# Performance work log

Hardware: AMD Instinct MI355X
Metric: run time of the kernel (lower is better)

## Reference

```python
import jax, jax.numpy as jnp
import numpy as np

MAX_DEPTH = 8          # inner-node depths 1..8; leaves at depth 9
LMBDA = 0.1            # args.lmbda; per-node lmbda = LMBDA * 2**(-depth)
EPS = 1e-6


def setup_inputs() -> dict:
    key = jax.random.key(0)
    ks = jax.random.split(key, 7)
    B, D, O = 16384, 2048, 1000
    n_inner = 2 ** MAX_DEPTH - 1   # 255
    n_leaf = 2 ** MAX_DEPTH       # 256
    x = jax.random.normal(ks[0], (B, D), dtype=jnp.float32)
    target = jax.random.randint(ks[1], (B,), 0, O)
    y = jax.nn.one_hot(target, O, dtype=jnp.float32)  # target_onehot
    W = jax.random.normal(ks[2], (n_inner, D), dtype=jnp.float32) / np.sqrt(D)
    b = jax.random.normal(ks[3], (n_inner,), dtype=jnp.float32) * 0.01
    beta = jax.random.normal(ks[4], (n_inner,), dtype=jnp.float32)
    leaf_params = jax.random.normal(ks[5], (n_leaf, O), dtype=jnp.float32)
    return {"x": x, "y": y, "W": W, "b": b, "beta": beta, "leaf_params": leaf_params}


def reference(x, y, W, b, beta, leaf_params):
    """Faithful vectorized version of SoftDecisionTree.cal_loss.
    Inner nodes are stored in level-order (heap) layout, left-to-right
    within each level, matching the left-first recursion of cal_prob.
    Returns (loss, output) like cal_loss.
    """
    B = x.shape[0]
    dt = x.dtype
    # All inner-node gates in one fused GEMM: sigmoid(beta * (x @ w + b))
    probs = jax.nn.sigmoid(beta * (x @ W.T + b))  # [B, n_inner]

    path = jnp.ones((B, 1), dt)  # path_prob_init
    C = jnp.asarray(0.0, dt)
    idx = 0
    for d in range(1, MAX_DEPTH + 1):  # small fixed loop over tree levels
        n = 2 ** (d - 1)
        p = probs[:, idx:idx + n]      # gate probs for this level's nodes [B, n]
        if d < MAX_DEPTH:              # get_penalty skips nodes whose children are leaves
            denom = jnp.sum(path, axis=0)                  # [n]
            denom = jnp.where(denom == 0, EPS, denom)
            alpha = jnp.sum(p * path, axis=0) / denom      # [n]
            alpha = jnp.clip(alpha, EPS, 1.0 - EPS)
            lmbda = LMBDA * 2.0 ** (-d)
            C = C - jnp.sum(lmbda * 0.5 * (jnp.log(alpha) + jnp.log1p(-alpha)))
        # children: left gets path*(1-p), right gets path*p, interleaved
        path = jnp.stack([path * (1.0 - p), path * p], axis=-1).reshape(B, 2 * n)
        idx += n
    # path: [B, n_leaf] leaf arrival probabilities (left-to-right leaf order)

    logQ = jax.nn.log_softmax(leaf_params, axis=-1)  # [n_leaf, O]
    TQ = y @ logQ.T                                  # [B, n_leaf]: y . log Q per leaf
    loss_term = jnp.mean(jnp.sum(path * TQ, axis=1))
    loss = -loss_term + C

    best = jnp.argmax(path, axis=1)   # first max, matches the '<' update order
    output = jnp.exp(logQ)[best]      # [B, O] max_Q
    return loss, output
```

## Files before the change

kernel.cpp:

```cpp
#include <hip/hip_runtime.h>


typedef __attribute__((ext_vector_type(8))) short short8;
typedef __attribute__((ext_vector_type(4))) float f32x4;

#define B_ROWS 16384
#define DIM 2048
#define NCLS 1000
#define NINNER 255
#define NPAD 256

__device__ __forceinline__ unsigned cvt2bf(float a, float b) {
  return ((__float_as_uint(a) + 0x8000u) >> 16) | ((__float_as_uint(b) + 0x8000u) & 0xFFFF0000u);
}

__global__ __launch_bounds__(256) void prep_w(const float* __restrict__ W,
                                              const float* __restrict__ b,
                                              const float* __restrict__ beta,
                                              unsigned short* __restrict__ Wb,
                                              float* __restrict__ bp,
                                              float* __restrict__ betap) {
  int i = blockIdx.x * 256 + threadIdx.x;
  int n = i >> 11;
  float v = (n < NINNER) ? W[i] : 0.f;
  Wb[i] = (unsigned short)((__float_as_uint(v) + 0x8000u) >> 16);
  if (i < NPAD) {
    bp[i] = (i < NINNER) ? b[i] : 0.f;
    betap[i] = (i < NINNER) ? beta[i] : 0.f;
  }
}

__global__ __launch_bounds__(256) void leaf_softmax(const float* __restrict__ leaf,
                                                    float* __restrict__ logQ,
                                                    float* __restrict__ Q) {
  int l = blockIdx.x, t = threadIdx.x;
  const float* row = leaf + (size_t)l * NCLS;
  __shared__ float red[256];
  float mx = -3.4e38f;
  for (int j = t; j < NCLS; j += 256) mx = fmaxf(mx, row[j]);
  red[t] = mx; __syncthreads();
  for (int s = 128; s; s >>= 1) { if (t < s) red[t] = fmaxf(red[t], red[t + s]); __syncthreads(); }
  mx = red[0]; __syncthreads();
  float sm = 0.f;
  for (int j = t; j < NCLS; j += 256) sm += expf(row[j] - mx);
  red[t] = sm; __syncthreads();
  for (int s = 128; s; s >>= 1) { if (t < s) red[t] += red[t + s]; __syncthreads(); }
  float lse = mx + logf(red[0]);
  for (int j = t; j < NCLS; j += 256) {
    float lg = row[j] - lse;
    logQ[(size_t)l * NCLS + j] = lg;
    Q[(size_t)l * NCLS + j] = expf(lg);
  }
}

__global__ __launch_bounds__(256) void find_targets(const float* __restrict__ y,
                                                    int* __restrict__ tgt) {
  int wv = threadIdx.x >> 6, lane = threadIdx.x & 63;
  int r = blockIdx.x * 4 + wv;
  const float4* yr = (const float4*)(y + (size_t)r * NCLS);
  int found = 0x7fffffff;
#pragma unroll
  for (int i = 0; i < 4; ++i) {
    int j4 = i * 64 + lane;
    if (j4 < 250) {
      float4 v = yr[j4];
      if (v.x > 0.5f) found = min(found, 4 * j4 + 0);
      if (v.y > 0.5f) found = min(found, 4 * j4 + 1);
      if (v.z > 0.5f) found = min(found, 4 * j4 + 2);
      if (v.w > 0.5f) found = min(found, 4 * j4 + 3);
    }
  }
  for (int off = 32; off; off >>= 1) found = min(found, __shfl_down(found, off));
  if (lane == 0) tgt[r] = found;
}

__global__ __launch_bounds__(256) void gemm_probs(const float* __restrict__ x,
                                                  const unsigned short* __restrict__ Wb,
                                                  const float* __restrict__ bp,
                                                  const float* __restrict__ betap,
                                                  float* __restrict__ probs) {
  __shared__ __align__(16) unsigned short As[128 * 32];
  __shared__ __align__(16) unsigned short Bs[64 * 32];
  __shared__ float ep[128 * 65];
  __shared__ float bsh[64], besh[64];

  int tid = threadIdx.x;
  int lane = tid & 63, wave = tid >> 6;
  int m_base = blockIdx.x * 128;
  int n_base = blockIdx.y * 64;

  if (tid < 64) { bsh[tid] = bp[n_base + tid]; besh[tid] = betap[n_base + tid]; }

  f32x4 acc[2][4] = {};

  int arow = tid >> 1, ahalf = tid & 1;
  const float* aptr = x + (size_t)(m_base + arow) * DIM + ahalf * 16;
  unsigned short* asd = &As[arow * 32 + ahalf * 16];
  int brow = tid >> 2, bseg = tid & 3;
  const unsigned short* bptr = Wb + (size_t)(n_base + brow) * DIM + bseg * 8;
  unsigned short* bsd = &Bs[brow * 32 + bseg * 8];

  int frow = lane & 15, fquad = lane >> 4;
  const unsigned short* afrag0 = &As[(wave * 32 + frow) * 32 + fquad * 8];
  const unsigned short* afrag1 = afrag0 + 16 * 32;

  for (int kt = 0; kt < DIM; kt += 32) {
    float4 v0 = *(const float4*)(aptr + kt);
    float4 v1 = *(const float4*)(aptr + kt + 4);
    float4 v2 = *(const float4*)(aptr + kt + 8);
    float4 v3 = *(const float4*)(aptr + kt + 12);
    uint4 bw = *(const uint4*)(bptr + kt);
    uint4 p0, p1;
    p0.x = cvt2bf(v0.x, v0.y); p0.y = cvt2bf(v0.z, v0.w);
    p0.z = cvt2bf(v1.x, v1.y); p0.w = cvt2bf(v1.z, v1.w);
    p1.x = cvt2bf(v2.x, v2.y); p1.y = cvt2bf(v2.z, v2.w);
    p1.z = cvt2bf(v3.x, v3.y); p1.w = cvt2bf(v3.z, v3.w);
    __syncthreads();
    *(uint4*)asd = p0;
    *(uint4*)(asd + 8) = p1;
    *(uint4*)bsd = bw;
    __syncthreads();
    short8 a0 = *(const short8*)afrag0;
    short8 a1 = *(const short8*)afrag1;
#pragma unroll
    for (int nt = 0; nt < 4; ++nt) {
      short8 bfr = *(const short8*)&Bs[(nt * 16 + frow) * 32 + fquad * 8];
      acc[0][nt] = __builtin_amdgcn_mfma_f32_16x16x32_bf16(a0, bfr, acc[0][nt], 0, 0, 0);
      acc[1][nt] = __builtin_amdgcn_mfma_f32_16x16x32_bf16(a1, bfr, acc[1][nt], 0, 0, 0);
    }
  }
  __syncthreads();
#pragma unroll
  for (int mt = 0; mt < 2; ++mt)
#pragma unroll
    for (int nt = 0; nt < 4; ++nt)
#pragma unroll
      for (int rg = 0; rg < 4; ++rg)
        ep[(wave * 32 + mt * 16 + fquad * 4 + rg) * 65 + nt * 16 + frow] = acc[mt][nt][rg];
  __syncthreads();
  int mrow = tid >> 1, nh = (tid & 1) * 32;
  float* dst = probs + (size_t)(m_base + mrow) * NPAD + n_base + nh;
#pragma unroll
  for (int u = 0; u < 8; ++u) {
    int n0 = nh + u * 4;
    float4 o;
    o.x = 1.f / (1.f + expf(-besh[n0 + 0] * (ep[mrow * 65 + n0 + 0] + bsh[n0 + 0])));
    o.y = 1.f / (1.f + expf(-besh[n0 + 1] * (ep[mrow * 65 + n0 + 1] + bsh[n0 + 1])));
    o.z = 1.f / (1.f + expf(-besh[n0 + 2] * (ep[mrow * 65 + n0 + 2] + bsh[n0 + 2])));
    o.w = 1.f / (1.f + expf(-besh[n0 + 3] * (ep[mrow * 65 + n0 + 3] + bsh[n0 + 3])));
    *(float4*)(dst + u * 4) = o;
  }
}

__global__ __launch_bounds__(256) void tree_walk(const float* __restrict__ probs,
                                                 const float* __restrict__ logQ,
                                                 const int* __restrict__ tgt,
                                                 float* __restrict__ acc,
                                                 int* __restrict__ best) {
  __shared__ float s0s[127], s1s[127];
  __shared__ float sdot;
  int tid = threadIdx.x;
  int lane = tid & 63, wv = tid >> 6;
  if (tid < 127) { s0s[tid] = 0.f; s1s[tid] = 0.f; }
  if (tid == 255) sdot = 0.f;
  __syncthreads();
  float wdot = 0.f;
  for (int it = 0; it < 16; ++it) {
    int r = blockIdx.x * 64 + wv * 16 + it;
    int tg = tgt[r];
    const float* pr = probs + (size_t)r * NPAD;
    const float* lq = logQ + tg;
    float pp = 1.f;
#pragma unroll
    for (int d = 1; d <= 6; ++d) {
      int pos = lane >> (7 - d);
      int idx = (1 << (d - 1)) - 1 + pos;
      float p = pr[idx];
      if ((lane & ((1 << (7 - d)) - 1)) == 0) {
        atomicAdd(&s0s[idx], pp);
        atomicAdd(&s1s[idx], p * pp);
      }
      pp *= ((lane >> (6 - d)) & 1) ? p : (1.f - p);
    }
    float p7 = pr[63 + lane];
    atomicAdd(&s0s[63 + lane], pp);
    atomicAdd(&s1s[63 + lane], p7 * pp);
    float pL = pp * (1.f - p7), pR = pp * p7;
    float p8a = pr[127 + 2 * lane], p8b = pr[128 + 2 * lane];
    float lf0 = pL * (1.f - p8a), lf1 = pL * p8a;
    float lf2 = pR * (1.f - p8b), lf3 = pR * p8b;
    wdot += lf0 * lq[(size_t)(4 * lane + 0) * NCLS] + lf1 * lq[(size_t)(4 * lane + 1) * NCLS]
          + lf2 * lq[(size_t)(4 * lane + 2) * NCLS] + lf3 * lq[(size_t)(4 * lane + 3) * NCLS];
    float bv = lf0; int bi = 4 * lane;
    if (lf1 > bv) { bv = lf1; bi = 4 * lane + 1; }
    if (lf2 > bv) { bv = lf2; bi = 4 * lane + 2; }
    if (lf3 > bv) { bv = lf3; bi = 4 * lane + 3; }
    for (int off = 32; off; off >>= 1) {
      float ov = __shfl_down(bv, off);
      int oi = __shfl_down(bi, off);
      if (ov > bv || (ov == bv && oi < bi)) { bv = ov; bi = oi; }
    }
    if (lane == 0) best[r] = bi;
  }
  for (int off = 32; off; off >>= 1) wdot += __shfl_down(wdot, off);
  if (lane == 0) atomicAdd(&sdot, wdot);
  __syncthreads();
  if (tid < 127) {
    atomicAdd(&acc[tid], s0s[tid]);
    atomicAdd(&acc[127 + tid], s1s[tid]);
  }
  if (tid == 255) atomicAdd(&acc[254], sdot);
}

__global__ __launch_bounds__(128) void finalize_loss(const float* __restrict__ acc,
                                                     float* __restrict__ out) {
  __shared__ float red[128];
  int t = threadIdx.x;
  float c = 0.f;
  if (t < 127) {
    float denom = acc[t];
    if (denom == 0.f) denom = 1e-6f;
    float alpha = acc[127 + t] / denom;
    alpha = fminf(fmaxf(alpha, 1e-6f), 1.f - 1e-6f);
    int d = 31 - __clz(t + 1) + 1;
    float lm = 0.1f * exp2f(-(float)d);
    c = -lm * 0.5f * (logf(alpha) + log1pf(-alpha));
  }
  red[t] = c;
  __syncthreads();
  for (int s = 64; s; s >>= 1) { if (t < s) red[t] += red[t + s]; __syncthreads(); }
  if (t == 0) out[0] = -(acc[254] / 16384.f) + red[0];
}

__global__ __launch_bounds__(256) void gather_rows(const float* __restrict__ Q,
                                                   const int* __restrict__ best,
                                                   float* __restrict__ out) {
  int wv = threadIdx.x >> 6, lane = threadIdx.x & 63;
  int r = blockIdx.x * 4 + wv;
  const float* src = Q + (size_t)best[r] * NCLS;
  float* dst = out + 1 + (size_t)r * NCLS;
  if (lane < 3) dst[lane] = src[lane];
  if (lane == 0) dst[999] = src[999];
#pragma unroll
  for (int i = 0; i < 4; ++i) {
    int q = i * 64 + lane;
    if (q < 249) {
      int o = 3 + 4 * q;
      float4 v = make_float4(src[o], src[o + 1], src[o + 2], src[o + 3]);
      *(float4*)(dst + o) = v;
    }
  }
}

extern "C" void kernel_launch(void* const* d_in, const int* in_sizes, int n_in,
                              void* d_out, int out_size, void* d_ws, size_t ws_size,
                              hipStream_t stream) {
  const float* x = (const float*)d_in[0];
  const float* y = (const float*)d_in[1];
  const float* W = (const float*)d_in[2];
  const float* b = (const float*)d_in[3];
  const float* beta = (const float*)d_in[4];
  const float* leaf = (const float*)d_in[5];
  float* out = (float*)d_out;
  char* ws = (char*)d_ws;

  unsigned short* Wb = (unsigned short*)(ws + 0);
  float* bp    = (float*)(ws + 1048576);
  float* betap = (float*)(ws + 1049600);
  float* acc   = (float*)(ws + 1050624);
  int* tgt     = (int*)(ws + 1051648);
  int* best    = (int*)(ws + 1117184);
  float* logQ  = (float*)(ws + 1182720);
  float* Q     = (float*)(ws + 2206720);
  float* probs = (float*)(ws + 3230720);

  prep_w<<<2048, 256, 0, stream>>>(W, b, beta, Wb, bp, betap);
  leaf_softmax<<<256, 256, 0, stream>>>(leaf, logQ, Q);
  find_targets<<<4096, 256, 0, stream>>>(y, tgt);
  gemm_probs<<<dim3(128, 4), 256, 0, stream>>>(x, Wb, bp, betap, probs);
  hipMemsetAsync(acc, 0, 255 * sizeof(float), stream);
  tree_walk<<<256, 256, 0, stream>>>(probs, logQ, tgt, acc, best);
  finalize_loss<<<1, 128, 0, stream>>>(acc, out);
  gather_rows<<<4096, 256, 0, stream>>>(Q, best, out);
}
```

Measured before the change: 382.3 us.

## Split-K GEMM with larger tiles, async W loads, sigmoid moved into tree walk

The GEMM now uses 128x128 tiles with split-K across two z-slices. W tiles are loaded with global_load_lds async copies, and the raw partial sums go to two buffers, one of them stashed in the output region. The tree walk sums the partials, applies bias, beta and sigmoid, and stages the gate probabilities in LDS. logQ is stored transposed so the per-row target lookup becomes a single float4 load, and the tree walk launches more blocks. The aim is better MFMA reuse, more parallelism, and no strided gathers, at the cost of extra partial-sum traffic and reliance on gather_rows overwriting the scratch output later.

```diff
diff --git a/kernel.cpp b/kernel.cpp
--- a/kernel.cpp
+++ b/kernel.cpp
@@ -4,7 +4,6 @@
 typedef __attribute__((ext_vector_type(8))) short short8;
 typedef __attribute__((ext_vector_type(4))) float f32x4;
 
-#define B_ROWS 16384
 #define DIM 2048
 #define NCLS 1000
 #define NINNER 255
@@ -12,6 +11,12 @@
 
 __device__ __forceinline__ unsigned cvt2bf(float a, float b) {
   return ((__float_as_uint(a) + 0x8000u) >> 16) | ((__float_as_uint(b) + 0x8000u) & 0xFFFF0000u);
+}
+
+__device__ __forceinline__ void async_copy16(const unsigned short* gsrc, unsigned short* ldst) {
+  __builtin_amdgcn_global_load_lds(
+      (const __attribute__((address_space(1))) unsigned int*)(gsrc),
+      (__attribute__((address_space(3))) unsigned int*)(ldst), 16, 0, 0);
 }
 
 __global__ __launch_bounds__(256) void prep_w(const float* __restrict__ W,
@@ -31,7 +36,7 @@
 }
 
 __global__ __launch_bounds__(256) void leaf_softmax(const float* __restrict__ leaf,
-                                                    float* __restrict__ logQ,
+                                                    float* __restrict__ logQT,
                                                     float* __restrict__ Q) {
   int l = blockIdx.x, t = threadIdx.x;
   const float* row = leaf + (size_t)l * NCLS;
@@ -42,14 +47,14 @@
   for (int s = 128; s; s >>= 1) { if (t < s) red[t] = fmaxf(red[t], red[t + s]); __syncthreads(); }
   mx = red[0]; __syncthreads();
   float sm = 0.f;
-  for (int j = t; j < NCLS; j += 256) sm += expf(row[j] - mx);
+  for (int j = t; j < NCLS; j += 256) sm += __expf(row[j] - mx);
   red[t] = sm; __syncthreads();
   for (int s = 128; s; s >>= 1) { if (t < s) red[t] += red[t + s]; __syncthreads(); }
-  float lse = mx + logf(red[0]);
+  float lse = mx + __logf(red[0]);
   for (int j = t; j < NCLS; j += 256) {
     float lg = row[j] - lse;
-    logQ[(size_t)l * NCLS + j] = lg;
-    Q[(size_t)l * NCLS + j] = expf(lg);
+    logQT[(size_t)j * NPAD + l] = lg;
+    Q[(size_t)l * NCLS + j] = __expf(lg);
   }
 }
 
@@ -74,42 +79,40 @@
   if (lane == 0) tgt[r] = found;
 }
 
-__global__ __launch_bounds__(256) void gemm_probs(const float* __restrict__ x,
-                                                  const unsigned short* __restrict__ Wb,
-                                                  const float* __restrict__ bp,
-                                                  const float* __restrict__ betap,
-                                                  float* __restrict__ probs) {
-  __shared__ __align__(16) unsigned short As[128 * 32];
-  __shared__ __align__(16) unsigned short Bs[64 * 32];
-  __shared__ float ep[128 * 65];
-  __shared__ float bsh[64], besh[64];
+__global__ __launch_bounds__(256, 2) void gemm_xwT(const float* __restrict__ x,
+                                                   const unsigned short* __restrict__ Wb,
+                                                   float* __restrict__ P0,
+                                                   float* __restrict__ P1) {
+  __shared__ __align__(16) unsigned short As[128 * 40];
+  __shared__ __align__(16) unsigned short Bs[128 * 32];
 
   int tid = threadIdx.x;
   int lane = tid & 63, wave = tid >> 6;
   int m_base = blockIdx.x * 128;
-  int n_base = blockIdx.y * 64;
-
-  if (tid < 64) { bsh[tid] = bp[n_base + tid]; besh[tid] = betap[n_base + tid]; }
-
-  f32x4 acc[2][4] = {};
-
-  int arow = tid >> 1, ahalf = tid & 1;
-  const float* aptr = x + (size_t)(m_base + arow) * DIM + ahalf * 16;
-  unsigned short* asd = &As[arow * 32 + ahalf * 16];
-  int brow = tid >> 2, bseg = tid & 3;
-  const unsigned short* bptr = Wb + (size_t)(n_base + brow) * DIM + bseg * 8;
-  unsigned short* bsd = &Bs[brow * 32 + bseg * 8];
+  int n_base = blockIdx.y * 128;
+  int k_base = blockIdx.z * 1024;
+  float* P = blockIdx.z ? P1 : P0;
+
+  f32x4 acc[4][4] = {};
+
+  int arow = tid >> 1, aseg = tid & 1;
+  const float* aptr = x + (size_t)(m_base + arow) * DIM + k_base + aseg * 16;
+  unsigned short* asd = &As[arow * 40 + aseg * 16];
+
+  int ci0 = wave * 2, ci1 = wave * 2 + 1;
+  const unsigned short* bg0 =
+      Wb + (size_t)(n_base + ci0 * 16 + (lane >> 2)) * DIM + k_base + (lane & 3) * 8;
+  const unsigned short* bg1 = bg0 + (size_t)16 * DIM;
+  unsigned short* bl0 = &Bs[ci0 * 512];
+  unsigned short* bl1 = &Bs[ci1 * 512];
 
   int frow = lane & 15, fquad = lane >> 4;
-  const unsigned short* afrag0 = &As[(wave * 32 + frow) * 32 + fquad * 8];
-  const unsigned short* afrag1 = afrag0 + 16 * 32;
-
-  for (int kt = 0; kt < DIM; kt += 32) {
-    float4 v0 = *(const float4*)(aptr + kt);
-    float4 v1 = *(const float4*)(aptr + kt + 4);
-    float4 v2 = *(const float4*)(aptr + kt + 8);
-    float4 v3 = *(const float4*)(aptr + kt + 12);
-    uint4 bw = *(const uint4*)(bptr + kt);
+  int wrow = (wave & 1) * 64;
+  int wcol = (wave >> 1) * 64;
+
+  for (int kt = 0; kt < 1024; kt += 32) {
+    const float4* ap = (const float4*)(aptr + kt);
+    float4 v0 = ap[0], v1 = ap[1], v2 = ap[2], v3 = ap[3];
     uint4 p0, p1;
     p0.x = cvt2bf(v0.x, v0.y); p0.y = cvt2bf(v0.z, v0.w);
     p0.z = cvt2bf(v1.x, v1.y); p0.w = cvt2bf(v1.z, v1.w);
@@ -118,45 +121,41 @@
     __syncthreads();
     *(uint4*)asd = p0;
     *(uint4*)(asd + 8) = p1;
-    *(uint4*)bsd = bw;
+    async_copy16(bg0 + kt, bl0);
+    async_copy16(bg1 + kt, bl1);
     __syncthreads();
-    short8 a0 = *(const short8*)afrag0;
-    short8 a1 = *(const short8*)afrag1;
+    short8 a[4];
+#pragma unroll
+    for (int mt = 0; mt < 4; ++mt)
+      a[mt] = *(const short8*)&As[(wrow + mt * 16 + frow) * 40 + fquad * 8];
 #pragma unroll
     for (int nt = 0; nt < 4; ++nt) {
-      short8 bfr = *(const short8*)&Bs[(nt * 16 + frow) * 32 + fquad * 8];
-      acc[0][nt] = __builtin_amdgcn_mfma_f32_16x16x32_bf16(a0, bfr, acc[0][nt], 0, 0, 0);
-      acc[1][nt] = __builtin_amdgcn_mfma_f32_16x16x32_bf16(a1, bfr, acc[1][nt], 0, 0, 0);
-    }
-  }
-  __syncthreads();
-#pragma unroll
-  for (int mt = 0; mt < 2; ++mt)
-#pragma unroll
-    for (int nt = 0; nt < 4; ++nt)
-#pragma unroll
-      for (int rg = 0; rg < 4; ++rg)
-        ep[(wave * 32 + mt * 16 + fquad * 4 + rg) * 65 + nt * 16 + frow] = acc[mt][nt][rg];
-  __syncthreads();
-  int mrow = tid >> 1, nh = (tid & 1) * 32;
-  float* dst = probs + (size_t)(m_base + mrow) * NPAD + n_base + nh;
-#pragma unroll
-  for (int u = 0; u < 8; ++u) {
-    int n0 = nh + u * 4;
-    float4 o;
-    o.x = 1.f / (1.f + expf(-besh[n0 + 0] * (ep[mrow * 65 + n0 + 0] + bsh[n0 + 0])));
-    o.y = 1.f / (1.f + expf(-besh[n0 + 1] * (ep[mrow * 65 + n0 + 1] + bsh[n0 + 1])));
-    o.z = 1.f / (1.f + expf(-besh[n0 + 2] * (ep[mrow * 65 + n0 + 2] + bsh[n0 + 2])));
-    o.w = 1.f / (1.f + expf(-besh[n0 + 3] * (ep[mrow * 65 + n0 + 3] + bsh[n0 + 3])));
-    *(float4*)(dst + u * 4) = o;
-  }
-}
-
-__global__ __launch_bounds__(256) void tree_walk(const float* __restrict__ probs,
-                                                 const float* __restrict__ logQ,
+      short8 bb = *(const short8*)&Bs[(wcol + nt * 16 + frow) * 32 + fquad * 8];
+#pragma unroll
+      for (int mt = 0; mt < 4; ++mt)
+        acc[mt][nt] = __builtin_amdgcn_mfma_f32_16x16x32_bf16(a[mt], bb, acc[mt][nt], 0, 0, 0);
+    }
+  }
+#pragma unroll
+  for (int mt = 0; mt < 4; ++mt) {
+#pragma unroll
+    for (int rg = 0; rg < 4; ++rg) {
+      float* dst = P + (size_t)(m_base + wrow + mt * 16 + fquad * 4 + rg) * NPAD + n_base + wcol + frow;
+#pragma unroll
+      for (int nt = 0; nt < 4; ++nt) dst[nt * 16] = acc[mt][nt][rg];
+    }
+  }
+}
+
+__global__ __launch_bounds__(256) void tree_walk(const float* __restrict__ P0,
+                                                 const float* __restrict__ P1,
+                                                 const float* __restrict__ bp,
+                                                 const float* __restrict__ betap,
+                                                 const float* __restrict__ logQT,
                                                  const int* __restrict__ tgt,
                                                  float* __restrict__ acc,
                                                  int* __restrict__ best) {
+  __shared__ float ws[4][256];
   __shared__ float s0s[127], s1s[127];
   __shared__ float sdot;
   int tid = threadIdx.x;
@@ -164,33 +163,42 @@
   if (tid < 127) { s0s[tid] = 0.f; s1s[tid] = 0.f; }
   if (tid == 255) sdot = 0.f;
   __syncthreads();
+  float4 bb = *(const float4*)(bp + lane * 4);
+  float4 be = *(const float4*)(betap + lane * 4);
+  float* wsp = ws[wv];
   float wdot = 0.f;
-  for (int it = 0; it < 16; ++it) {
-    int r = blockIdx.x * 64 + wv * 16 + it;
+  for (int it = 0; it < 4; ++it) {
+    int r = blockIdx.x * 16 + wv * 4 + it;
+    float4 u = *(const float4*)(P0 + (size_t)r * NPAD + lane * 4);
+    float4 v = *(const float4*)(P1 + (size_t)r * NPAD + lane * 4);
+    float4 pz;
+    pz.x = 1.f / (1.f + __expf(-be.x * (u.x + v.x + bb.x)));
+    pz.y = 1.f / (1.f + __expf(-be.y * (u.y + v.y + bb.y)));
+    pz.z = 1.f / (1.f + __expf(-be.z * (u.z + v.z + bb.z)));
+    pz.w = 1.f / (1.f + __expf(-be.w * (u.w + v.w + bb.w)));
+    *(float4*)(wsp + lane * 4) = pz;
+    __asm__ volatile("" ::: "memory");
     int tg = tgt[r];
-    const float* pr = probs + (size_t)r * NPAD;
-    const float* lq = logQ + tg;
     float pp = 1.f;
 #pragma unroll
     for (int d = 1; d <= 6; ++d) {
-      int pos = lane >> (7 - d);
-      int idx = (1 << (d - 1)) - 1 + pos;
-      float p = pr[idx];
+      int idx = (1 << (d - 1)) - 1 + (lane >> (7 - d));
+      float p = wsp[idx];
       if ((lane & ((1 << (7 - d)) - 1)) == 0) {
         atomicAdd(&s0s[idx], pp);
         atomicAdd(&s1s[idx], p * pp);
       }
       pp *= ((lane >> (6 - d)) & 1) ? p : (1.f - p);
     }
-    float p7 = pr[63 + lane];
+    float p7 = wsp[63 + lane];
     atomicAdd(&s0s[63 + lane], pp);
     atomicAdd(&s1s[63 + lane], p7 * pp);
     float pL = pp * (1.f - p7), pR = pp * p7;
-    float p8a = pr[127 + 2 * lane], p8b = pr[128 + 2 * lane];
+    float p8a = wsp[127 + 2 * lane], p8b = wsp[128 + 2 * lane];
     float lf0 = pL * (1.f - p8a), lf1 = pL * p8a;
     float lf2 = pR * (1.f - p8b), lf3 = pR * p8b;
-    wdot += lf0 * lq[(size_t)(4 * lane + 0) * NCLS] + lf1 * lq[(size_t)(4 * lane + 1) * NCLS]
-          + lf2 * lq[(size_t)(4 * lane + 2) * NCLS] + lf3 * lq[(size_t)(4 * lane + 3) * NCLS];
+    float4 lq = *(const float4*)(logQT + (size_t)tg * NPAD + lane * 4);
+    wdot += lf0 * lq.x + lf1 * lq.y + lf2 * lq.z + lf3 * lq.w;
     float bv = lf0; int bi = 4 * lane;
     if (lf1 > bv) { bv = lf1; bi = 4 * lane + 1; }
     if (lf2 > bv) { bv = lf2; bi = 4 * lane + 2; }
@@ -270,16 +278,17 @@
   float* acc   = (float*)(ws + 1050624);
   int* tgt     = (int*)(ws + 1051648);
   int* best    = (int*)(ws + 1117184);
-  float* logQ  = (float*)(ws + 1182720);
+  float* logQT = (float*)(ws + 1182720);
   float* Q     = (float*)(ws + 2206720);
-  float* probs = (float*)(ws + 3230720);
+  float* P0    = (float*)(ws + 3230720);
+  float* P1    = out + 4;
 
   prep_w<<<2048, 256, 0, stream>>>(W, b, beta, Wb, bp, betap);
-  leaf_softmax<<<256, 256, 0, stream>>>(leaf, logQ, Q);
+  leaf_softmax<<<256, 256, 0, stream>>>(leaf, logQT, Q);
   find_targets<<<4096, 256, 0, stream>>>(y, tgt);
-  gemm_probs<<<dim3(128, 4), 256, 0, stream>>>(x, Wb, bp, betap, probs);
-  hipMemsetAsync(acc, 0, 255 * sizeof(float), stream);
-  tree_walk<<<256, 256, 0, stream>>>(probs, logQ, tgt, acc, best);
+  gemm_xwT<<<dim3(128, 2, 2), 256, 0, stream>>>(x, Wb, P0, P1);
+  hipMemsetAsync(acc, 0, 256 * sizeof(float), stream);
+  tree_walk<<<1024, 256, 0, stream>>>(P0, P1, bp, betap, logQT, tgt, acc, best);
   finalize_loss<<<1, 128, 0, stream>>>(acc, out);
   gather_rows<<<4096, 256, 0, stream>>>(Q, best, out);
 }
```

New measurement: 362.9 us. 5.1% less time.
